# Performance work log

Measured on AMD Instinct MI355X. Metric: run time of the kernel, lower is better.

## Reference

```python
import jax, jax.numpy as jnp
import numpy as np

B, C, H, W, N = 16, 81, 128, 128, 64


def setup_inputs() -> dict:
    key = jax.random.key(0)
    k1, k2, k3, k4, k5 = jax.random.split(key, 5)
    bbox_pred = jax.random.normal(k1, (B, 4, H, W), jnp.float32)
    class_pred = jax.random.normal(k2, (B, C, H, W), jnp.float32)
    # well-formed GT boxes in [0,1]: x1y1 + positive wh
    xy = jax.random.uniform(k3, (B, N, 2), jnp.float32)
    wh = jax.random.uniform(k4, (B, N, 2), jnp.float32) * 0.5 + 0.05
    boxes = jnp.concatenate([xy, xy + wh], axis=-1)  # [B,N,4]
    labels = jax.random.randint(k5, (B, N), 0, C).astype(jnp.int32)
    return {"bbox_pred": bbox_pred, "class_pred": class_pred,
            "boxes": boxes, "labels": labels}


def reference(bbox_pred, class_pred, boxes, labels):
    Bb, Cc, Hh, Ww = class_pred.shape
    A = Hh * Ww
    pb = bbox_pred.transpose(0, 2, 3, 1).reshape(Bb, A, 4)   # [B,A,4]
    pc = class_pred.transpose(0, 2, 3, 1).reshape(Bb, A, Cc)  # [B,A,C]

    # pairwise IoU [B,A,N] via broadcasting (pred [B,A,1,4] vs gt [B,1,N,4])
    p = pb[:, :, None, :]
    g = boxes[:, None, :, :]
    ix1 = jnp.maximum(p[..., 0], g[..., 0])
    iy1 = jnp.maximum(p[..., 1], g[..., 1])
    ix2 = jnp.minimum(p[..., 2], g[..., 2])
    iy2 = jnp.minimum(p[..., 3], g[..., 3])
    inter = jnp.clip(ix2 - ix1, 0) * jnp.clip(iy2 - iy1, 0)
    pa = (pb[..., 2] - pb[..., 0]) * (pb[..., 3] - pb[..., 1])      # [B,A]
    ga = (boxes[..., 2] - boxes[..., 0]) * (boxes[..., 3] - boxes[..., 1])  # [B,N]
    union = pa[:, :, None] + ga[:, None, :] - inter
    ious = inter / union

    max_ious = ious.max(axis=-1)            # [B,A]
    max_idx = jnp.argmax(ious, axis=-1)     # [B,A]
    pos = max_ious > 0.5                    # [B,A]
    posf = pos.astype(pc.dtype)
    npos = posf.sum(axis=-1)                # [B]
    denom = jnp.maximum(npos, 1.0)

    assigned_labels = jnp.take_along_axis(labels, max_idx, axis=1)          # [B,A]
    assigned_boxes = jnp.take_along_axis(boxes, max_idx[..., None], axis=1)  # [B,A,4]

    # cross-entropy per anchor (mean over positives)
    logp = jax.nn.log_softmax(pc, axis=-1)
    ce = -jnp.take_along_axis(logp, assigned_labels[..., None], axis=2)[..., 0]
    cls_loss = (ce * posf).sum(axis=-1) / denom

    # smooth-L1 (beta=1), mean over positive elements (npos*4)
    diff = pb - assigned_boxes
    ad = jnp.abs(diff)
    sl1 = jnp.where(ad < 1.0, 0.5 * diff * diff, ad - 0.5)
    reg_loss = (sl1 * posf[..., None]).sum(axis=(-1, -2)) / (denom * 4.0)

    # fallback when an image has zero positives: CE with all-zero labels
    zero_loss = -logp[..., 0].mean(axis=-1)

    per_img = jnp.where(npos > 0, cls_loss + reg_loss, zero_loss)
    return per_img.mean()
```

## Files before the change

kernel.cpp:

```cpp
#include <hip/hip_runtime.h>
#include <math.h>

#define Bc 16
#define Cc 81
#define AA 16384
#define Nn 64
#define TPB 512
#define BLOCKS_PER_IMG (AA / TPB)
#define NBLOCKS (Bc * BLOCKS_PER_IMG)
#define G 9
#define NG 9

__global__ __launch_bounds__(TPB) void det_loss_main(
    const float* __restrict__ bbox_pred,
    const float* __restrict__ class_pred,
    const float* __restrict__ boxes,
    const int* __restrict__ labels,
    float4* __restrict__ ws_part)
{
    __shared__ float4 sbox[Nn];
    __shared__ float  sga[Nn];
    __shared__ int    slab[Nn];

    const int blk  = blockIdx.x;
    const int b    = blk / BLOCKS_PER_IMG;
    const int ablk = blk % BLOCKS_PER_IMG;
    const int t    = threadIdx.x;

    if (t < Nn) {
        float4 g = ((const float4*)boxes)[b * Nn + t];
        sbox[t] = g;
        sga[t]  = (g.z - g.x) * (g.w - g.y);
        slab[t] = labels[b * Nn + t];
    }
    __syncthreads();

    const int a = ablk * TPB + t;

    const float* bp = bbox_pred + (size_t)b * 4 * AA + a;
    const float px1 = bp[0 * AA];
    const float py1 = bp[1 * AA];
    const float px2 = bp[2 * AA];
    const float py2 = bp[3 * AA];
    const float pa  = (px2 - px1) * (py2 - py1);

    const float* cp = class_pred + (size_t)b * Cc * AA + a;
    float buf0[G], buf1[G], buf2[G];
#pragma unroll
    for (int k = 0; k < G; ++k) buf0[k] = cp[(size_t)(0 * G + k) * AA];
#pragma unroll
    for (int k = 0; k < G; ++k) buf1[k] = cp[(size_t)(1 * G + k) * AA];

    float best = -INFINITY;
    int   bj   = 0;
#pragma unroll 8
    for (int j = 0; j < Nn; ++j) {
        const float4 g  = sbox[j];
        const float ix1 = fmaxf(px1, g.x);
        const float iy1 = fmaxf(py1, g.y);
        const float ix2 = fminf(px2, g.z);
        const float iy2 = fminf(py2, g.w);
        const float inter = fmaxf(ix2 - ix1, 0.0f) * fmaxf(iy2 - iy1, 0.0f);
        const float iou = inter * __builtin_amdgcn_rcpf(pa + sga[j] - inter);
        if (iou > best) { best = iou; bj = j; }
    }
    const float posf = (best > 0.5f) ? 1.0f : 0.0f;
    const int    lab = slab[bj];
    const float4 gb  = sbox[bj];

    float sA = 0.0f, sB = 0.0f, x0 = 0.0f, xl = 0.0f;
#pragma unroll
    for (int g = 0; g < NG; ++g) {
        if (g + 2 < NG) {
            const int m = (g + 2) % 3;
            if (m == 0) {
#pragma unroll
                for (int k = 0; k < G; ++k) buf0[k] = cp[(size_t)((g + 2) * G + k) * AA];
            } else if (m == 1) {
#pragma unroll
                for (int k = 0; k < G; ++k) buf1[k] = cp[(size_t)((g + 2) * G + k) * AA];
            } else {
#pragma unroll
                for (int k = 0; k < G; ++k) buf2[k] = cp[(size_t)((g + 2) * G + k) * AA];
            }
        }
        const int mc = g % 3;
#pragma unroll
        for (int k = 0; k < G; ++k) {
            const float x = (mc == 0) ? buf0[k] : ((mc == 1) ? buf1[k] : buf2[k]);
            const int   c = g * G + k;
            if (c == 0) x0 = x;
            xl = (c == lab) ? x : xl;
            if (k & 1) sB += __expf(x);
            else       sA += __expf(x);
        }
    }
    const float lse   = __logf(sA + sB);
    const float ce    = (lse - xl) * posf;
    const float logp0 = x0 - lse;

    float sl = 0.0f;
    {
        const float d0 = px1 - gb.x, d1 = py1 - gb.y, d2 = px2 - gb.z, d3 = py2 - gb.w;
        const float a0 = fabsf(d0), a1 = fabsf(d1), a2 = fabsf(d2), a3 = fabsf(d3);
        sl += (a0 < 1.0f) ? 0.5f * d0 * d0 : a0 - 0.5f;
        sl += (a1 < 1.0f) ? 0.5f * d1 * d1 : a1 - 0.5f;
        sl += (a2 < 1.0f) ? 0.5f * d2 * d2 : a2 - 0.5f;
        sl += (a3 < 1.0f) ? 0.5f * d3 * d3 : a3 - 0.5f;
        sl *= posf;
    }

    float v0 = posf, v1 = ce, v2 = sl, v3 = logp0;
#pragma unroll
    for (int o = 32; o > 0; o >>= 1) {
        v0 += __shfl_down(v0, o);
        v1 += __shfl_down(v1, o);
        v2 += __shfl_down(v2, o);
        v3 += __shfl_down(v3, o);
    }
    __shared__ float4 red[8];
    const int wave = t >> 6, lane = t & 63;
    if (lane == 0) red[wave] = make_float4(v0, v1, v2, v3);
    __syncthreads();
    if (t == 0) {
        float4 s = red[0];
#pragma unroll
        for (int r = 1; r < 8; ++r) {
            s.x += red[r].x; s.y += red[r].y; s.z += red[r].z; s.w += red[r].w;
        }
        ws_part[blk] = s;
    }
}

__global__ __launch_bounds__(256) void det_loss_final(
    const float4* __restrict__ ws_part, float* __restrict__ out)
{
    const int t = threadIdx.x;
    float4 p0 = ws_part[t];
    float4 p1 = ws_part[t + 256];
#pragma unroll
    for (int o = 1; o < 32; o <<= 1) {
        p0.x += __shfl_xor(p0.x, o); p0.y += __shfl_xor(p0.y, o);
        p0.z += __shfl_xor(p0.z, o); p0.w += __shfl_xor(p0.w, o);
        p1.x += __shfl_xor(p1.x, o); p1.y += __shfl_xor(p1.y, o);
        p1.z += __shfl_xor(p1.z, o); p1.w += __shfl_xor(p1.w, o);
    }
    __shared__ float4 simg[16];
    const int lane = t & 63, w = t >> 6;
    if (lane == 0 || lane == 32) {
        const int img = 2 * w + (lane >> 5);
        simg[img]     = p0;
        simg[img + 8] = p1;
    }
    __syncthreads();
    float per = 0.0f;
    if (t < Bc) {
        const float4 s = simg[t];
        const float npos = s.x;
        const float denom = fmaxf(npos, 1.0f);
        const float cls_reg = s.y / denom + s.z / (denom * 4.0f);
        const float zero_loss = -s.w / (float)AA;
        per = (npos > 0.0f) ? cls_reg : zero_loss;
    }
#pragma unroll
    for (int o = 8; o > 0; o >>= 1) per += __shfl_down(per, o);
    if (t == 0) out[0] = per * (1.0f / (float)Bc);
}

extern "C" void kernel_launch(void* const* d_in, const int* in_sizes, int n_in,
                              void* d_out, int out_size, void* d_ws, size_t ws_size,
                              hipStream_t stream) {
    const float* bbox_pred  = (const float*)d_in[0];
    const float* class_pred = (const float*)d_in[1];
    const float* boxes      = (const float*)d_in[2];
    const int*   labels     = (const int*)d_in[3];
    float* out = (float*)d_out;
    float4* ws = (float4*)d_ws;

    det_loss_main<<<NBLOCKS, TPB, 0, stream>>>(bbox_pred, class_pred, boxes, labels, ws);
    det_loss_final<<<1, 256, 0, stream>>>(ws, out);
}
```

Before: 24.03 us.

## Fuse final reduction into main kernel via atomics and last-block detection

Replaces the separate finalize kernel with per-image atomic accumulation and a global counter, so the last block to finish computes the final loss. The workspace is zeroed with a memset before launch. The first barrier also moves after the initial class-logit loads so those loads are issued earlier. This removes one kernel launch and the dependency gap between kernels, at the cost of a memset, atomic contention on 64 floats, and nondeterministic floating-point summation order.

```diff
diff --git a/kernel.cpp b/kernel.cpp
--- a/kernel.cpp
+++ b/kernel.cpp
@@ -11,16 +11,22 @@
 #define G 9
 #define NG 9
 
-__global__ __launch_bounds__(TPB) void det_loss_main(
+#define WS_ZERO_BYTES 320
+
+__global__ __launch_bounds__(TPB) void det_loss_fused(
     const float* __restrict__ bbox_pred,
     const float* __restrict__ class_pred,
     const float* __restrict__ boxes,
     const int* __restrict__ labels,
-    float4* __restrict__ ws_part)
+    float* __restrict__ acc,
+    unsigned int* __restrict__ counter,
+    float* __restrict__ out)
 {
     __shared__ float4 sbox[Nn];
     __shared__ float  sga[Nn];
     __shared__ int    slab[Nn];
+    __shared__ float4 red[8];
+    __shared__ int    s_islast;
 
     const int blk  = blockIdx.x;
     const int b    = blk / BLOCKS_PER_IMG;
@@ -33,7 +39,6 @@
         sga[t]  = (g.z - g.x) * (g.w - g.y);
         slab[t] = labels[b * Nn + t];
     }
-    __syncthreads();
 
     const int a = ablk * TPB + t;
 
@@ -50,6 +55,8 @@
     for (int k = 0; k < G; ++k) buf0[k] = cp[(size_t)(0 * G + k) * AA];
 #pragma unroll
     for (int k = 0; k < G; ++k) buf1[k] = cp[(size_t)(1 * G + k) * AA];
+
+    __syncthreads();
 
     float best = -INFINITY;
     int   bj   = 0;
@@ -118,7 +125,6 @@
         v2 += __shfl_down(v2, o);
         v3 += __shfl_down(v3, o);
     }
-    __shared__ float4 red[8];
     const int wave = t >> 6, lane = t & 63;
     if (lane == 0) red[wave] = make_float4(v0, v1, v2, v3);
     __syncthreads();
@@ -128,38 +134,28 @@
         for (int r = 1; r < 8; ++r) {
             s.x += red[r].x; s.y += red[r].y; s.z += red[r].z; s.w += red[r].w;
         }
-        ws_part[blk] = s;
-    }
-}
-
-__global__ __launch_bounds__(256) void det_loss_final(
-    const float4* __restrict__ ws_part, float* __restrict__ out)
-{
-    const int t = threadIdx.x;
-    float4 p0 = ws_part[t];
-    float4 p1 = ws_part[t + 256];
-#pragma unroll
-    for (int o = 1; o < 32; o <<= 1) {
-        p0.x += __shfl_xor(p0.x, o); p0.y += __shfl_xor(p0.y, o);
-        p0.z += __shfl_xor(p0.z, o); p0.w += __shfl_xor(p0.w, o);
-        p1.x += __shfl_xor(p1.x, o); p1.y += __shfl_xor(p1.y, o);
-        p1.z += __shfl_xor(p1.z, o); p1.w += __shfl_xor(p1.w, o);
-    }
-    __shared__ float4 simg[16];
-    const int lane = t & 63, w = t >> 6;
-    if (lane == 0 || lane == 32) {
-        const int img = 2 * w + (lane >> 5);
-        simg[img]     = p0;
-        simg[img + 8] = p1;
+        float* ai = acc + 4 * b;
+        atomicAdd(ai + 0, s.x);
+        atomicAdd(ai + 1, s.y);
+        atomicAdd(ai + 2, s.z);
+        atomicAdd(ai + 3, s.w);
+        asm volatile("s_waitcnt vmcnt(0)" ::: "memory");
+        const unsigned int c = atomicAdd(counter, 1u);
+        s_islast = (c == NBLOCKS - 1) ? 1 : 0;
     }
     __syncthreads();
+    if (!s_islast) return;
+
     float per = 0.0f;
     if (t < Bc) {
-        const float4 s = simg[t];
-        const float npos = s.x;
+        const float* ai = acc + 4 * t;
+        const float npos = __hip_atomic_load(ai + 0, __ATOMIC_RELAXED, __HIP_MEMORY_SCOPE_AGENT);
+        const float ces  = __hip_atomic_load(ai + 1, __ATOMIC_RELAXED, __HIP_MEMORY_SCOPE_AGENT);
+        const float sls  = __hip_atomic_load(ai + 2, __ATOMIC_RELAXED, __HIP_MEMORY_SCOPE_AGENT);
+        const float lp0  = __hip_atomic_load(ai + 3, __ATOMIC_RELAXED, __HIP_MEMORY_SCOPE_AGENT);
         const float denom = fmaxf(npos, 1.0f);
-        const float cls_reg = s.y / denom + s.z / (denom * 4.0f);
-        const float zero_loss = -s.w / (float)AA;
+        const float cls_reg = ces / denom + sls / (denom * 4.0f);
+        const float zero_loss = -lp0 / (float)AA;
         per = (npos > 0.0f) ? cls_reg : zero_loss;
     }
 #pragma unroll
@@ -175,8 +171,10 @@
     const float* boxes      = (const float*)d_in[2];
     const int*   labels     = (const int*)d_in[3];
     float* out = (float*)d_out;
-    float4* ws = (float4*)d_ws;
+    float* acc = (float*)d_ws;
+    unsigned int* counter = (unsigned int*)((char*)d_ws + 256);
 
-    det_loss_main<<<NBLOCKS, TPB, 0, stream>>>(bbox_pred, class_pred, boxes, labels, ws);
-    det_loss_final<<<1, 256, 0, stream>>>(ws, out);
+    hipMemsetAsync(d_ws, 0, WS_ZERO_BYTES, stream);
+    det_loss_fused<<<NBLOCKS, TPB, 0, stream>>>(bbox_pred, class_pred, boxes, labels,
+                                                acc, counter, out);
 }
```

After: 36.35 us. 51.2% more time.
